# Optimization experiments

Measured on AMD Instinct MI355X. Metric: run time of the kernel, lower is better.

The kernel has to match this reference:

```python
import jax, jax.numpy as jnp
import numpy as np

B, T, C, HR = 8, 4096, 256, 4
N_LAYER, LAYER_ID = 12, 3
HID = HR * C


def _fancy_decay_first():
    # Faithful reproduction of VRWKV_SpatialMix._init_weights(init_mode='fancy')
    r01 = LAYER_ID / (N_LAYER - 1)
    h = np.arange(C, dtype=np.float32)
    decay = -5.0 + 8.0 * (h / (C - 1)) ** (0.7 + 1.3 * r01)
    zig = ((np.arange(1, C + 1) % 3) - 1).astype(np.float32) * 0.5
    first = np.float32(np.log(0.3)) + zig
    return jnp.asarray(decay, jnp.float32), jnp.asarray(first, jnp.float32)


def setup_inputs() -> dict:
    key = jax.random.key(0)
    ks = jax.random.split(key, 12)
    s = 0.02  # small weight scale keeps exp(k) well-conditioned
    decay, first = _fancy_decay_first()
    return {
        "x": jax.random.normal(ks[0], (B, T, C), jnp.float32),
        "Wk": jax.random.normal(ks[1], (C, C), jnp.float32) * s,
        "Wv": jax.random.normal(ks[2], (C, C), jnp.float32) * s,
        "Wr": jax.random.normal(ks[3], (C, C), jnp.float32) * s,
        "Wo": jax.random.normal(ks[4], (C, C), jnp.float32) * s,
        "Wk_ffn": jax.random.normal(ks[5], (C, HID), jnp.float32) * s,
        "Wv_ffn": jax.random.normal(ks[6], (HID, C), jnp.float32) * s,
        "Wr_ffn": jax.random.normal(ks[7], (C, C), jnp.float32) * s,
        "g1": 1.0 + 0.1 * jax.random.normal(ks[8], (C,), jnp.float32),
        "b1": 0.1 * jax.random.normal(ks[9], (C,), jnp.float32),
        "g2": 1.0 + 0.1 * jax.random.normal(ks[10], (C,), jnp.float32),
        "b2": 0.1 * jax.random.normal(ks[11], (C,), jnp.float32),
        "spatial_decay": decay,
        "spatial_first": first,
    }


def _ln(x, g, b):
    m = jnp.mean(x, axis=-1, keepdims=True)
    v = jnp.var(x, axis=-1, keepdims=True)
    return (x - m) * jax.lax.rsqrt(v + 1e-5) * g + b


def _wkv(w, u, k, v):
    # Numerically-stable log-space WKV recurrence (same math as wkv_cuda):
    # y_t = (sum_{i<t} e^{w*(t-1-i)+k_i} v_i + e^{u+k_t} v_t)
    #     / (sum_{i<t} e^{w*(t-1-i)+k_i}     + e^{u+k_t})
    # w,u: [C]; k,v: [B,T,C] -> y: [B,T,C]
    Bb, Tt, Cc = k.shape
    kT = jnp.swapaxes(k, 0, 1)  # [T,B,C]
    vT = jnp.swapaxes(v, 0, 1)

    def step(carry, kv):
        p, q, o = carry           # [B,C] num / den / running max exponent
        kt, vt = kv               # [B,C]
        no = jnp.maximum(o, u + kt)
        A = jnp.exp(o - no)
        E = jnp.exp(u + kt - no)
        y = (A * p + E * vt) / (A * q + E)
        no2 = jnp.maximum(w + o, kt)
        A2 = jnp.exp(w + o - no2)
        E2 = jnp.exp(kt - no2)
        return (A2 * p + E2 * vt, A2 * q + E2, no2), y

    init = (jnp.zeros((Bb, Cc), k.dtype),
            jnp.zeros((Bb, Cc), k.dtype),
            jnp.full((Bb, Cc), -1e38, k.dtype))
    _, yT = jax.lax.scan(step, init, (kT, vT))
    return jnp.swapaxes(yT, 0, 1)


def reference(x, Wk, Wv, Wr, Wo, Wk_ffn, Wv_ffn, Wr_ffn, g1, b1, g2, b2,
              spatial_decay, spatial_first):
    Tlen = x.shape[1]
    # --- SpatialMix (shift_pixel=0 -> xk=xv=xr=h, key_norm=False) ---
    h = _ln(x, g1, b1)
    k = h @ Wk
    v = h @ Wv
    sr = jax.nn.sigmoid(h @ Wr)
    y = _wkv(spatial_decay / Tlen, spatial_first / Tlen, k, v)
    x = x + (sr * y) @ Wo
    # --- ChannelMix (square-ReLU MLP, sigmoid receptance gate) ---
    h2 = _ln(x, g2, b2)
    kk = jnp.square(jax.nn.relu(h2 @ Wk_ffn))
    x = x + jax.nn.sigmoid(h2 @ Wr_ffn) * (kk @ Wv_ffn)
    return x
```

## Files before the change

### kernel.cpp

```cpp
#include <hip/hip_runtime.h>
#include <hip/hip_bf16.h>
#include <math.h>

#define TDIM 4096
#define CDIM 256
#define BDIM 8
#define NTOK (BDIM * TDIM)
#define HIDDIM 1024
#define NCHUNK 128
#define CHLEN 32

typedef float f32x4 __attribute__((ext_vector_type(4)));
typedef __bf16 bf16x8 __attribute__((ext_vector_type(8)));
typedef __bf16 bf16x4 __attribute__((ext_vector_type(4)));

#define GLDS16(gp, lp) __builtin_amdgcn_global_load_lds( \
    (const __attribute__((address_space(1))) void*)(gp), \
    (__attribute__((address_space(3))) void*)(lp), 16, 0, 0)

#define WAITCNT_VM6 0x0F76
#define WAITCNT_VM4 0x0F74
#define WAITCNT_VM2 0x0F72
#define WAITCNT_VM0 0x0F70

__device__ __forceinline__ float sigm(float v) { return 1.0f / (1.0f + __expf(-v)); }

__global__ __launch_bounds__(256) void pack_weights(
    const float* __restrict__ Wk, const float* __restrict__ Wv,
    const float* __restrict__ Wr, const float* __restrict__ Wo,
    const float* __restrict__ Wkf, const float* __restrict__ Wvf,
    const float* __restrict__ Wrf,
    __bf16* __restrict__ WkvrT, __bf16* __restrict__ WoT,
    __bf16* __restrict__ Wkfr, unsigned char* __restrict__ Wvf8) {
  long long j = (long long)blockIdx.x * 256 + threadIdx.x;
  if (j < 196608) {
    int n = (int)(j >> 8), k = (int)(j & 255);
    const float* src = (n < 256) ? Wk : (n < 512 ? Wv : Wr);
    WkvrT[j] = (__bf16)src[k * 256 + (n & 255)];
    return;
  }
  j -= 196608;
  if (j < 65536) { int n = (int)(j >> 8), k = (int)(j & 255);
    WoT[j] = (__bf16)Wo[k * 256 + n]; return; }
  j -= 65536;
  if (j < 327680) { int n = (int)(j >> 8), k = (int)(j & 255);
    Wkfr[j] = (__bf16)(n < 1024 ? Wkf[(long long)k * 1024 + n]
                                : Wrf[k * 256 + (n - 1024)]);
    return; }
  j -= 327680;
  if (j < 65536) {
    const long long d = j * 4;
    const int n = (int)(d >> 10), k0 = (int)(d & 1023);
    int w = 0;
    w = __builtin_amdgcn_cvt_pk_fp8_f32(Wvf[(long long)k0 * 256 + n],
                                        Wvf[(long long)(k0 + 1) * 256 + n], w, false);
    w = __builtin_amdgcn_cvt_pk_fp8_f32(Wvf[(long long)(k0 + 2) * 256 + n],
                                        Wvf[(long long)(k0 + 3) * 256 + n], w, true);
    *(int*)&Wvf8[d] = w;
    return;
  }
}

__global__ __launch_bounds__(256) void ln_kernel(
    const float* __restrict__ x, const float* __restrict__ gamma,
    const float* __restrict__ beta, __bf16* __restrict__ h) {
  const int wave = threadIdx.x >> 6, lane = threadIdx.x & 63;
  const long long row = (long long)blockIdx.x * 4 + wave;
  const long long base = row * CDIM + lane * 4;
  const f32x4 v = *(const f32x4*)&x[base];
  float s = v[0] + v[1] + v[2] + v[3];
  float s2 = v[0]*v[0] + v[1]*v[1] + v[2]*v[2] + v[3]*v[3];
  #pragma unroll
  for (int o = 1; o < 64; o <<= 1) { s += __shfl_xor(s, o); s2 += __shfl_xor(s2, o); }
  const float mean = s * (1.0f / CDIM);
  const float var = s2 * (1.0f / CDIM) - mean * mean;
  const float rstd = rsqrtf(var + 1e-5f);
  const f32x4 g4 = *(const f32x4*)&gamma[lane * 4];
  const f32x4 b4 = *(const f32x4*)&beta[lane * 4];
  bf16x4 o;
  #pragma unroll
  for (int r = 0; r < 4; r++) o[r] = (__bf16)((v[r] - mean) * rstd * g4[r] + b4[r]);
  *(bf16x4*)&h[base] = o;
}

template <int BN, int EPI>
__global__ __launch_bounds__(256, 2) void gemm3(
    const __bf16* __restrict__ A, const __bf16* __restrict__ Bt,
    int M, int N,
    __bf16* __restrict__ outH, __bf16* __restrict__ outH2,
    unsigned char* __restrict__ outC,
    const float* __restrict__ srcF,
    const float* __restrict__ gammaP, const float* __restrict__ betaP) {
  constexpr int K = 256;
  constexpr int WNT = BN / 32;
  constexpr int NBC = BN / 64;
  __shared__ __bf16 sA[3][128 * 32];
  __shared__ __bf16 sB[3][BN * 32];
  __shared__ float redS[2][128], redQ[2][128];

  const int tid = threadIdx.x;
  const int wave = tid >> 6, lane = tid & 63;
  const int quad = lane >> 4, mrow = lane & 15;
  const long long bm = (long long)blockIdx.x * 128;
  const long long bn = (long long)blockIdx.y * BN;
  const int wm = (wave & 1) * 64, wn = (wave >> 1) * (BN / 2);

  const int lrow = lane >> 2;
  const int lk = (lane & 3) * 8;

  auto issue = [&](int g) {
    const int buf = g % 3;
    const long long k0 = (long long)g * 32;
    const int a0 = wave * 32;
    GLDS16(A + (bm + a0 + lrow) * (long long)K + k0 + lk, &sA[buf][a0 * 32]);
    GLDS16(A + (bm + a0 + 16 + lrow) * (long long)K + k0 + lk, &sA[buf][(a0 + 16) * 32]);
    #pragma unroll
    for (int bc = 0; bc < NBC; bc++) {
      const int r0 = wave * (BN / 4) + bc * 16;
      GLDS16(Bt + (bn + r0 + lrow) * (long long)K + k0 + lk, &sB[buf][r0 * 32]);
    }
  };

  f32x4 acc[4][WNT] = {};

  const int nit = K / 32;
  issue(0);
  issue(1);

  auto compute = [&](int i) {
    const int buf = i % 3;
    bf16x8 fa[4], fb[WNT];
    #pragma unroll
    for (int mt = 0; mt < 4; mt++)
      fa[mt] = *(const bf16x8*)&sA[buf][(wm + mt * 16 + mrow) * 32 + quad * 8];
    #pragma unroll
    for (int nt = 0; nt < WNT; nt++)
      fb[nt] = *(const bf16x8*)&sB[buf][(wn + nt * 16 + mrow) * 32 + quad * 8];
    #pragma unroll
    for (int mt = 0; mt < 4; mt++)
      #pragma unroll
      for (int nt = 0; nt < WNT; nt++)
        acc[mt][nt] = __builtin_amdgcn_mfma_f32_16x16x32_bf16(fb[nt], fa[mt], acc[mt][nt], 0, 0, 0);
  };

  #pragma unroll 1
  for (int i = 0; i < nit - 1; i++) {
    __builtin_amdgcn_s_waitcnt(BN == 256 ? WAITCNT_VM6 : WAITCNT_VM4);
    __builtin_amdgcn_s_barrier();
    if (i + 2 < nit) issue(i + 2);
    compute(i);
  }
  __builtin_amdgcn_s_waitcnt(WAITCNT_VM0);
  __builtin_amdgcn_s_barrier();
  compute(nit - 1);

  if (EPI == 1) {
    float sum[4] = {0, 0, 0, 0}, sq[4] = {0, 0, 0, 0};
    #pragma unroll
    for (int mt = 0; mt < 4; mt++) {
      #pragma unroll
      for (int nt = 0; nt < WNT; nt++) {
        const long long row = bm + wm + mt * 16 + mrow;
        const long long colb = wn + nt * 16 + quad * 4;
        acc[mt][nt] += *(const f32x4*)&srcF[row * 256 + colb];
        #pragma unroll
        for (int r = 0; r < 4; r++) {
          sum[mt] += acc[mt][nt][r];
          sq[mt] += acc[mt][nt][r] * acc[mt][nt][r];
        }
      }
    }
    #pragma unroll
    for (int mt = 0; mt < 4; mt++) {
      sum[mt] += __shfl_xor(sum[mt], 16); sq[mt] += __shfl_xor(sq[mt], 16);
      sum[mt] += __shfl_xor(sum[mt], 32); sq[mt] += __shfl_xor(sq[mt], 32);
    }
    const int wnh = wave >> 1;
    if (quad == 0) {
      #pragma unroll
      for (int mt = 0; mt < 4; mt++) {
        redS[wnh][wm + mt * 16 + mrow] = sum[mt];
        redQ[wnh][wm + mt * 16 + mrow] = sq[mt];
      }
    }
    __syncthreads();
    #pragma unroll
    for (int mt = 0; mt < 4; mt++) {
      const int rb = wm + mt * 16 + mrow;
      const float ts = redS[0][rb] + redS[1][rb];
      const float tq = redQ[0][rb] + redQ[1][rb];
      const float mean = ts * (1.0f / 256.0f);
      const float rstd = rsqrtf(tq * (1.0f / 256.0f) - mean * mean + 1e-5f);
      const long long row = bm + rb;
      #pragma unroll
      for (int nt = 0; nt < WNT; nt++) {
        const long long colb = wn + nt * 16 + quad * 4;
        const f32x4 g4 = *(const f32x4*)&gammaP[colb];
        const f32x4 b4 = *(const f32x4*)&betaP[colb];
        bf16x4 xo, ho;
        #pragma unroll
        for (int r = 0; r < 4; r++) {
          const float t = acc[mt][nt][r];
          xo[r] = (__bf16)t;
          ho[r] = (__bf16)((t - mean) * rstd * g4[r] + b4[r]);
        }
        *(bf16x4*)&outH[row * 256 + colb] = xo;
        *(bf16x4*)&outH2[row * 256 + colb] = ho;
      }
    }
    return;
  }

  #pragma unroll
  for (int mt = 0; mt < 4; mt++) {
    #pragma unroll
    for (int nt = 0; nt < WNT; nt++) {
      const long long row = bm + wm + mt * 16 + mrow;
      const int cloc = wn + nt * 16 + quad * 4;
      const long long colb = bn + cloc;
      const f32x4 a = acc[mt][nt];
      if (EPI == 0) {
        const int plane = blockIdx.y >> 1;
        __bf16* o = outH + (long long)plane * ((long long)M * 256);
        const long long c2 = colb & 255;
        bf16x4 v;
        if (plane == 2) {
          #pragma unroll
          for (int r = 0; r < 4; r++) v[r] = (__bf16)sigm(a[r]);
        } else {
          #pragma unroll
          for (int r = 0; r < 4; r++) v[r] = (__bf16)a[r];
        }
        *(bf16x4*)&o[row * 256 + c2] = v;
      } else if (EPI == 2) {
        if (blockIdx.y < 8) {
          float t0 = a[0] > 0.0f ? a[0] : 0.0f;
          float t1 = a[1] > 0.0f ? a[1] : 0.0f;
          float t2 = a[2] > 0.0f ? a[2] : 0.0f;
          float t3 = a[3] > 0.0f ? a[3] : 0.0f;
          int w = 0;
          w = __builtin_amdgcn_cvt_pk_fp8_f32(t0 * t0, t1 * t1, w, false);
          w = __builtin_amdgcn_cvt_pk_fp8_f32(t2 * t2, t3 * t3, w, true);
          *(int*)&outC[row * 1024 + colb] = w;
        } else {
          bf16x4 v;
          #pragma unroll
          for (int r = 0; r < 4; r++) v[r] = (__bf16)sigm(a[r]);
          *(bf16x4*)&outH2[row * 256 + (colb - 1024)] = v;
        }
      }
    }
  }
}

__global__ __launch_bounds__(256, 4) void gemm6(
    const unsigned char* __restrict__ A8, const unsigned char* __restrict__ B8,
    float* __restrict__ outF, const __bf16* __restrict__ srcH,
    const __bf16* __restrict__ gate) {
  __shared__ unsigned char sA[3][128 * 32];
  __shared__ unsigned char sB[3][128 * 32];
  const int tid = threadIdx.x;
  const int wave = tid >> 6, lane = tid & 63;
  const int quad = lane >> 4, mrow = lane & 15;
  const long long bm = (long long)blockIdx.x * 128;
  const long long bn = (long long)blockIdx.y * 128;
  const int wm = (wave & 1) * 64, wn = (wave >> 1) * 64;
  const int srow = lane >> 1;
  const int hs = (lane & 1) ^ ((lane >> 2) & 1);

  auto issue = [&](int g) {
    const int buf = g % 3;
    const long long k0 = (long long)g * 32;
    const int a0 = wave * 32;
    GLDS16(A8 + (bm + a0 + srow) * 1024LL + k0 + hs * 16, &sA[buf][a0 * 32]);
    GLDS16(B8 + (bn + a0 + srow) * 1024LL + k0 + hs * 16, &sB[buf][a0 * 32]);
  };

  f32x4 acc[4][4] = {};
  issue(0);
  issue(1);
  const int sw = (mrow >> 1) & 1;

  auto compute = [&](int i) {
    const int buf = i % 3;
    long long fa[4], fb[4];
    const int off = ((((quad >> 1) ^ sw) << 4) | ((quad & 1) << 3));
    #pragma unroll
    for (int mt = 0; mt < 4; mt++)
      fa[mt] = *(const long long*)&sA[buf][(wm + mt * 16 + mrow) * 32 + off];
    #pragma unroll
    for (int nt = 0; nt < 4; nt++)
      fb[nt] = *(const long long*)&sB[buf][(wn + nt * 16 + mrow) * 32 + off];
    #pragma unroll
    for (int mt = 0; mt < 4; mt++)
      #pragma unroll
      for (int nt = 0; nt < 4; nt++)
        acc[mt][nt] = __builtin_amdgcn_mfma_f32_16x16x32_fp8_fp8(fb[nt], fa[mt], acc[mt][nt], 0, 0, 0);
  };

  #pragma unroll 1
  for (int i = 0; i < 31; i++) {
    __builtin_amdgcn_s_waitcnt(WAITCNT_VM2);
    __builtin_amdgcn_s_barrier();
    if (i + 2 < 32) issue(i + 2);
    compute(i);
  }
  __builtin_amdgcn_s_waitcnt(WAITCNT_VM0);
  __builtin_amdgcn_s_barrier();
  compute(31);

  #pragma unroll
  for (int mt = 0; mt < 4; mt++) {
    #pragma unroll
    for (int nt = 0; nt < 4; nt++) {
      const long long row = bm + wm + mt * 16 + mrow;
      const long long colb = bn + wn + nt * 16 + quad * 4;
      const long long idx = row * 256 + colb;
      const f32x4 a = acc[mt][nt];
      const bf16x4 s4 = *(const bf16x4*)&srcH[idx];
      const bf16x4 g4 = *(const bf16x4*)&gate[idx];
      f32x4 v;
      #pragma unroll
      for (int r = 0; r < 4; r++) v[r] = (float)s4[r] + (float)g4[r] * a[r];
      *(f32x4*)&outF[idx] = v;
    }
  }
}

__global__ __launch_bounds__(256) void wkv_phase1(
    const __bf16* __restrict__ ka, const __bf16* __restrict__ va,
    const float* __restrict__ decay,
    float* __restrict__ Sloc, float* __restrict__ Zloc) {
  const int wave = threadIdx.x >> 6, lane = threadIdx.x & 63;
  const int gi = blockIdx.x * 4 + wave;
  const int b = gi >> 7, chunk = gi & (NCHUNK - 1);
  const int c0 = lane * 4;
  const f32x4 w4 = *(const f32x4*)&decay[c0];
  f32x4 ew;
  #pragma unroll
  for (int r = 0; r < 4; r++) ew[r] = __expf(w4[r] * (1.0f / TDIM));
  f32x4 S = {0,0,0,0}, Z = {0,0,0,0};
  long long base = ((long long)b * TDIM + (long long)chunk * CHLEN) * 256 + c0;
  #pragma unroll 4
  for (int t = 0; t < CHLEN; t++) {
    const bf16x4 k4 = *(const bf16x4*)&ka[base + (long long)t * 256];
    const bf16x4 v4 = *(const bf16x4*)&va[base + (long long)t * 256];
    #pragma unroll
    for (int r = 0; r < 4; r++) {
      const float ek = __expf((float)k4[r]);
      S[r] = ew[r] * S[r] + ek * (float)v4[r];
      Z[r] = ew[r] * Z[r] + ek;
    }
  }
  const long long o = (long long)gi * 256 + c0;
  *(f32x4*)&Sloc[o] = S;
  *(f32x4*)&Zloc[o] = Z;
}

__global__ __launch_bounds__(256) void wkv_phase2(
    const float* __restrict__ Sloc, const float* __restrict__ Zloc,
    const float* __restrict__ decay,
    float* __restrict__ Sstart, float* __restrict__ Zstart) {
  const int idx = blockIdx.x * 256 + threadIdx.x;
  const int c = idx & 255;
  const int b = idx >> 8;
  const float w = decay[c] * (1.0f / TDIM);
  const float ewL = __expf(w * (float)CHLEN);
  float S = 0.0f, Z = 0.0f;
  for (int j = 0; j < NCHUNK; j++) {
    const long long o = ((long long)b * NCHUNK + j) * 256 + c;
    Sstart[o] = S;
    Zstart[o] = Z;
    S = ewL * S + Sloc[o];
    Z = ewL * Z + Zloc[o];
  }
}

__global__ __launch_bounds__(256) void wkv_phase3(
    const __bf16* __restrict__ ka, const __bf16* __restrict__ va,
    const __bf16* __restrict__ ra,
    const float* __restrict__ decay, const float* __restrict__ first,
    const float* __restrict__ Sstart, const float* __restrict__ Zstart,
    __bf16* __restrict__ a2) {
  const int wave = threadIdx.x >> 6, lane = threadIdx.x & 63;
  const int gi = blockIdx.x * 4 + wave;
  const int b = gi >> 7, chunk = gi & (NCHUNK - 1);
  const int c0 = lane * 4;
  const f32x4 w4 = *(const f32x4*)&decay[c0];
  const f32x4 u4 = *(const f32x4*)&first[c0];
  f32x4 ew, eu;
  #pragma unroll
  for (int r = 0; r < 4; r++) {
    ew[r] = __expf(w4[r] * (1.0f / TDIM));
    eu[r] = __expf(u4[r] * (1.0f / TDIM));
  }
  const long long so = (long long)gi * 256 + c0;
  f32x4 S = *(const f32x4*)&Sstart[so];
  f32x4 Z = *(const f32x4*)&Zstart[so];
  long long base = ((long long)b * TDIM + (long long)chunk * CHLEN) * 256 + c0;
  #pragma unroll 2
  for (int t = 0; t < CHLEN; t++) {
    const long long p = base + (long long)t * 256;
    const bf16x4 k4 = *(const bf16x4*)&ka[p];
    const bf16x4 v4 = *(const bf16x4*)&va[p];
    const bf16x4 r4 = *(const bf16x4*)&ra[p];
    bf16x4 o;
    #pragma unroll
    for (int r = 0; r < 4; r++) {
      const float ek = __expf((float)k4[r]);
      const float E = eu[r] * ek;
      const float y = (S[r] + E * (float)v4[r]) / (Z[r] + E);
      o[r] = (__bf16)((float)r4[r] * y);
      S[r] = ew[r] * S[r] + ek * (float)v4[r];
      Z[r] = ew[r] * Z[r] + ek;
    }
    *(bf16x4*)&a2[p] = o;
  }
}

extern "C" void kernel_launch(void* const* d_in, const int* in_sizes, int n_in,
                              void* d_out, int out_size, void* d_ws, size_t ws_size,
                              hipStream_t stream) {
  const float* x     = (const float*)d_in[0];
  const float* Wk    = (const float*)d_in[1];
  const float* Wv    = (const float*)d_in[2];
  const float* Wr    = (const float*)d_in[3];
  const float* Wo    = (const float*)d_in[4];
  const float* Wkf   = (const float*)d_in[5];
  const float* Wvf   = (const float*)d_in[6];
  const float* Wrf   = (const float*)d_in[7];
  const float* g1    = (const float*)d_in[8];
  const float* b1    = (const float*)d_in[9];
  const float* g2    = (const float*)d_in[10];
  const float* b2    = (const float*)d_in[11];
  const float* decay = (const float*)d_in[12];
  const float* first = (const float*)d_in[13];
  float* out = (float*)d_out;
  char* ws = (char*)d_ws;

  __bf16* ka     = (__bf16*)(ws + 0);
  __bf16* va     = (__bf16*)(ws + 16777216LL);
  __bf16* ra     = (__bf16*)(ws + 33554432LL);
  __bf16* a2     = (__bf16*)(ws + 50331648LL);
  __bf16* g2buf  = (__bf16*)(ws + 50331648LL);
  __bf16* hbuf   = (__bf16*)(ws + 67108864LL);
  __bf16* h2     = (__bf16*)(ws + 67108864LL);
  __bf16* x1h    = (__bf16*)(ws + 83886080LL);
  float*  Sloc   = (float*)(ws + 100663296LL);
  float*  Zloc   = (float*)(ws + 101711872LL);
  float*  Sstart = (float*)(ws + 102760448LL);
  float*  Zstart = (float*)(ws + 103809024LL);
  unsigned char* kk8 = (unsigned char*)(ws + 100663296LL);
  __bf16* WkvrT  = (__bf16*)(ws + 167772160LL);
  __bf16* WoT    = (__bf16*)(ws + 168165376LL);
  __bf16* Wkfr   = (__bf16*)(ws + 168296448LL);
  unsigned char* Wvf8 = (unsigned char*)(ws + 168951808LL);

  pack_weights<<<2560, 256, 0, stream>>>(Wk, Wv, Wr, Wo, Wkf, Wvf, Wrf,
                                         WkvrT, WoT, Wkfr, Wvf8);

  ln_kernel<<<NTOK / 4, 256, 0, stream>>>(x, g1, b1, hbuf);
  gemm3<128, 0><<<dim3(NTOK / 128, 6), 256, 0, stream>>>(
      hbuf, WkvrT, NTOK, 768, ka, nullptr, nullptr, nullptr, nullptr, nullptr);
  wkv_phase1<<<BDIM * NCHUNK / 4, 256, 0, stream>>>(ka, va, decay, Sloc, Zloc);
  wkv_phase2<<<BDIM, 256, 0, stream>>>(Sloc, Zloc, decay, Sstart, Zstart);
  wkv_phase3<<<BDIM * NCHUNK / 4, 256, 0, stream>>>(ka, va, ra, decay, first,
                                                    Sstart, Zstart, a2);
  gemm3<256, 1><<<dim3(NTOK / 128, 1), 256, 0, stream>>>(
      a2, WoT, NTOK, 256, x1h, h2, nullptr, x, g2, b2);

  gemm3<128, 2><<<dim3(NTOK / 128, 10), 256, 0, stream>>>(
      h2, Wkfr, NTOK, 1280, nullptr, g2buf, kk8, nullptr, nullptr, nullptr);
  gemm6<<<dim3(NTOK / 128, 2), 256, 0, stream>>>(
      kk8, Wvf8, out, x1h, g2buf);
}
```

Before: 278.6 us.

## Process multiple M tiles per GEMM block with continuous cross-tile prefetch pipeline

The bf16 GEMM kernel now loops over MT consecutive 128-row tiles per block, keeping the triple-buffered global-to-LDS pipeline running across tile boundaries so the next tile's loads overlap the current tile's epilogue and prologue. The epilogue runs inline after each tile and resets the accumulators. The QKV GEMM uses 2 tiles per block and the FFN key/receptance GEMM uses 4. Launch bounds are raised to 3 blocks per SM. This targets the per-block pipeline fill/drain and launch overhead, at the cost of fewer blocks (less parallelism) and more register pressure under the tighter occupancy bound.

```diff
diff --git a/kernel.cpp b/kernel.cpp
--- a/kernel.cpp
+++ b/kernel.cpp
@@ -18,10 +18,11 @@
     (const __attribute__((address_space(1))) void*)(gp), \
     (__attribute__((address_space(3))) void*)(lp), 16, 0, 0)
 
-#define WAITCNT_VM6 0x0F76
-#define WAITCNT_VM4 0x0F74
-#define WAITCNT_VM2 0x0F72
-#define WAITCNT_VM0 0x0F70
+#define WAITCNT_VM6  0x0F76
+#define WAITCNT_VM4  0x0F74
+#define WAITCNT_VM2  0x0F72
+#define WAITCNT_VM0  0x0F70
+#define WAITCNT_VM20 0x4F74
 
 __device__ __forceinline__ float sigm(float v) { return 1.0f / (1.0f + __expf(-v)); }
 
@@ -83,8 +84,8 @@
   *(bf16x4*)&h[base] = o;
 }
 
-template <int BN, int EPI>
-__global__ __launch_bounds__(256, 2) void gemm3(
+template <int BN, int EPI, int MT>
+__global__ __launch_bounds__(256, 3) void gemm3(
     const __bf16* __restrict__ A, const __bf16* __restrict__ Bt,
     int M, int N,
     __bf16* __restrict__ outH, __bf16* __restrict__ outH2,
@@ -101,7 +102,7 @@
   const int tid = threadIdx.x;
   const int wave = tid >> 6, lane = tid & 63;
   const int quad = lane >> 4, mrow = lane & 15;
-  const long long bm = (long long)blockIdx.x * 128;
+  const long long bm = (long long)blockIdx.x * (128 * MT);
   const long long bn = (long long)blockIdx.y * BN;
   const int wm = (wave & 1) * 64, wn = (wave >> 1) * (BN / 2);
 
@@ -110,10 +111,11 @@
 
   auto issue = [&](int g) {
     const int buf = g % 3;
-    const long long k0 = (long long)g * 32;
+    const long long k0 = (long long)(g & 7) * 32;
+    const long long ar = bm + (long long)(g >> 3) * 128;
     const int a0 = wave * 32;
-    GLDS16(A + (bm + a0 + lrow) * (long long)K + k0 + lk, &sA[buf][a0 * 32]);
-    GLDS16(A + (bm + a0 + 16 + lrow) * (long long)K + k0 + lk, &sA[buf][(a0 + 16) * 32]);
+    GLDS16(A + (ar + a0 + lrow) * (long long)K + k0 + lk, &sA[buf][a0 * 32]);
+    GLDS16(A + (ar + a0 + 16 + lrow) * (long long)K + k0 + lk, &sA[buf][(a0 + 16) * 32]);
     #pragma unroll
     for (int bc = 0; bc < NBC; bc++) {
       const int r0 = wave * (BN / 4) + bc * 16;
@@ -123,12 +125,8 @@
 
   f32x4 acc[4][WNT] = {};
 
-  const int nit = K / 32;
-  issue(0);
-  issue(1);
-
-  auto compute = [&](int i) {
-    const int buf = i % 3;
+  auto compute = [&](int g) {
+    const int buf = g % 3;
     bf16x8 fa[4], fb[WNT];
     #pragma unroll
     for (int mt = 0; mt < 4; mt++)
@@ -143,16 +141,68 @@
         acc[mt][nt] = __builtin_amdgcn_mfma_f32_16x16x32_bf16(fb[nt], fa[mt], acc[mt][nt], 0, 0, 0);
   };
 
+  auto epilogue = [&](int mti) {
+    const long long rb0 = bm + (long long)mti * 128;
+    #pragma unroll
+    for (int mt = 0; mt < 4; mt++) {
+      #pragma unroll
+      for (int nt = 0; nt < WNT; nt++) {
+        const long long row = rb0 + wm + mt * 16 + mrow;
+        const int cloc = wn + nt * 16 + quad * 4;
+        const long long colb = bn + cloc;
+        const f32x4 a = acc[mt][nt];
+        if (EPI == 0) {
+          const int plane = blockIdx.y >> 1;
+          __bf16* o = outH + (long long)plane * ((long long)M * 256);
+          const long long c2 = colb & 255;
+          bf16x4 v;
+          if (plane == 2) {
+            #pragma unroll
+            for (int r = 0; r < 4; r++) v[r] = (__bf16)sigm(a[r]);
+          } else {
+            #pragma unroll
+            for (int r = 0; r < 4; r++) v[r] = (__bf16)a[r];
+          }
+          *(bf16x4*)&o[row * 256 + c2] = v;
+        } else if (EPI == 2) {
+          if (blockIdx.y < 8) {
+            float t0 = a[0] > 0.0f ? a[0] : 0.0f;
+            float t1 = a[1] > 0.0f ? a[1] : 0.0f;
+            float t2 = a[2] > 0.0f ? a[2] : 0.0f;
+            float t3 = a[3] > 0.0f ? a[3] : 0.0f;
+            int w = 0;
+            w = __builtin_amdgcn_cvt_pk_fp8_f32(t0 * t0, t1 * t1, w, false);
+            w = __builtin_amdgcn_cvt_pk_fp8_f32(t2 * t2, t3 * t3, w, true);
+            *(int*)&outC[row * 1024 + colb] = w;
+          } else {
+            bf16x4 v;
+            #pragma unroll
+            for (int r = 0; r < 4; r++) v[r] = (__bf16)sigm(a[r]);
+            *(bf16x4*)&outH2[row * 256 + (colb - 1024)] = v;
+          }
+        }
+        acc[mt][nt] = (f32x4){0.0f, 0.0f, 0.0f, 0.0f};
+      }
+    }
+  };
+
+  constexpr int total = 8 * MT;
+  issue(0);
+  issue(1);
+
   #pragma unroll 1
-  for (int i = 0; i < nit - 1; i++) {
-    __builtin_amdgcn_s_waitcnt(BN == 256 ? WAITCNT_VM6 : WAITCNT_VM4);
+  for (int g = 0; g < total; g++) {
+    if (g == total - 1)
+      __builtin_amdgcn_s_waitcnt(WAITCNT_VM0);
+    else if (MT > 1 && g >= 8 && (g & 7) <= 1)
+      __builtin_amdgcn_s_waitcnt(WAITCNT_VM20);
+    else
+      __builtin_amdgcn_s_waitcnt(BN == 256 ? WAITCNT_VM6 : WAITCNT_VM4);
     __builtin_amdgcn_s_barrier();
-    if (i + 2 < nit) issue(i + 2);
-    compute(i);
-  }
-  __builtin_amdgcn_s_waitcnt(WAITCNT_VM0);
-  __builtin_amdgcn_s_barrier();
-  compute(nit - 1);
+    if (g + 2 < total) issue(g + 2);
+    compute(g);
+    if (EPI != 1 && (g & 7) == 7) epilogue(g >> 3);
+  }
 
   if (EPI == 1) {
     float sum[4] = {0, 0, 0, 0}, sq[4] = {0, 0, 0, 0};
@@ -206,48 +256,6 @@
         }
         *(bf16x4*)&outH[row * 256 + colb] = xo;
         *(bf16x4*)&outH2[row * 256 + colb] = ho;
-      }
-    }
-    return;
-  }
-
-  #pragma unroll
-  for (int mt = 0; mt < 4; mt++) {
-    #pragma unroll
-    for (int nt = 0; nt < WNT; nt++) {
-      const long long row = bm + wm + mt * 16 + mrow;
-      const int cloc = wn + nt * 16 + quad * 4;
-      const long long colb = bn + cloc;
-      const f32x4 a = acc[mt][nt];
-      if (EPI == 0) {
-        const int plane = blockIdx.y >> 1;
-        __bf16* o = outH + (long long)plane * ((long long)M * 256);
-        const long long c2 = colb & 255;
-        bf16x4 v;
-        if (plane == 2) {
-          #pragma unroll
-          for (int r = 0; r < 4; r++) v[r] = (__bf16)sigm(a[r]);
-        } else {
-          #pragma unroll
-          for (int r = 0; r < 4; r++) v[r] = (__bf16)a[r];
-        }
-        *(bf16x4*)&o[row * 256 + c2] = v;
-      } else if (EPI == 2) {
-        if (blockIdx.y < 8) {
-          float t0 = a[0] > 0.0f ? a[0] : 0.0f;
-          float t1 = a[1] > 0.0f ? a[1] : 0.0f;
-          float t2 = a[2] > 0.0f ? a[2] : 0.0f;
-          float t3 = a[3] > 0.0f ? a[3] : 0.0f;
-          int w = 0;
-          w = __builtin_amdgcn_cvt_pk_fp8_f32(t0 * t0, t1 * t1, w, false);
-          w = __builtin_amdgcn_cvt_pk_fp8_f32(t2 * t2, t3 * t3, w, true);
-          *(int*)&outC[row * 1024 + colb] = w;
-        } else {
-          bf16x4 v;
-          #pragma unroll
-          for (int r = 0; r < 4; r++) v[r] = (__bf16)sigm(a[r]);
-          *(bf16x4*)&outH2[row * 256 + (colb - 1024)] = v;
-        }
       }
     }
   }
@@ -460,16 +468,16 @@
                                          WkvrT, WoT, Wkfr, Wvf8);
 
   ln_kernel<<<NTOK / 4, 256, 0, stream>>>(x, g1, b1, hbuf);
-  gemm3<128, 0><<<dim3(NTOK / 128, 6), 256, 0, stream>>>(
+  gemm3<128, 0, 2><<<dim3(NTOK / 256, 6), 256, 0, stream>>>(
       hbuf, WkvrT, NTOK, 768, ka, nullptr, nullptr, nullptr, nullptr, nullptr);
   wkv_phase1<<<BDIM * NCHUNK / 4, 256, 0, stream>>>(ka, va, decay, Sloc, Zloc);
   wkv_phase2<<<BDIM, 256, 0, stream>>>(Sloc, Zloc, decay, Sstart, Zstart);
   wkv_phase3<<<BDIM * NCHUNK / 4, 256, 0, stream>>>(ka, va, ra, decay, first,
                                                     Sstart, Zstart, a2);
-  gemm3<256, 1><<<dim3(NTOK / 128, 1), 256, 0, stream>>>(
+  gemm3<256, 1, 1><<<dim3(NTOK / 128, 1), 256, 0, stream>>>(
       a2, WoT, NTOK, 256, x1h, h2, nullptr, x, g2, b2);
 
-  gemm3<128, 2><<<dim3(NTOK / 128, 10), 256, 0, stream>>>(
+  gemm3<128, 2, 4><<<dim3(NTOK / 512, 10), 256, 0, stream>>>(
       h2, Wkfr, NTOK, 1280, nullptr, g2buf, kk8, nullptr, nullptr, nullptr);
   gemm6<<<dim3(NTOK / 128, 2), 256, 0, stream>>>(
       kk8, Wvf8, out, x1h, g2buf);
```

Result: slower. 287.4 us (+3.1%).
